# Performance work log

Measured on AMD Instinct MI355X. Metric: run time of the kernel, lower is better.

Reference implementation:

```python
import jax, jax.numpy as jnp
import numpy as np

EPS = 1e-06


def setup_inputs() -> dict:
    key = jax.random.key(0)
    k0, k1, k2, k3 = jax.random.split(key, 4)
    N = 4096  # num_gaussians (64**2)
    H = W = 128
    # Gaussian centers in [-1, 1]^2 (matches the init position grid range)
    position = jax.random.uniform(k0, (1, N, 2), minval=-1.0, maxval=1.0, dtype=jnp.float32)
    # Module stores color = raw_colors + 1 and subtracts 1 at the end of forward
    color = jax.random.uniform(k1, (1, N, 3), dtype=jnp.float32) + 1.0
    # Module init is log_scale = -5; use -3 +/- noise so kernels have visible support
    log_scale = jax.random.normal(k2, (1, N, 2), dtype=jnp.float32) * 0.5 - 3.0
    rotation = jax.random.normal(k3, (1, N), dtype=jnp.float32) * 0.5
    alphas = jnp.ones((1, N), dtype=jnp.float32)
    return dict(position=position, color=color, log_scale=log_scale,
                rotation=rotation, alphas=alphas, height=H, width=W, num_active=N)


def reference(position, color, log_scale, rotation, alphas, height, width, num_active):
    """2D anisotropic Gaussian splat render (dense per-pixel evaluation).

    For every pixel p and gaussian g: rotate the offset into the gaussian
    frame, evaluate exp(-0.5 * quadratic form), weight by alpha and
    accumulate color.  Output [1, 3, H, W] minus 1 (module returns render-1).
    """
    n = num_active
    pos = position[0, :n]                       # [N, 2]
    col = color[0, :n]                          # [N, 3]
    scale = jnp.exp(log_scale[0, :n]) + EPS     # [N, 2]
    rot = rotation[0, :n]                       # [N]
    alph = alphas[0, :n]                        # [N]

    # Pixel grid in [-1, 1], x along width, y along height
    xs = jnp.linspace(-1.0, 1.0, width, dtype=pos.dtype)
    ys = jnp.linspace(-1.0, 1.0, height, dtype=pos.dtype)
    x_grid, y_grid = jnp.meshgrid(xs, ys)       # each [H, W]
    P = height * width
    px = x_grid.reshape(P, 1)                   # [P, 1]
    py = y_grid.reshape(P, 1)

    dx = px - pos[None, :, 0]                   # [P, N]
    dy = py - pos[None, :, 1]                   # [P, N]
    c = jnp.cos(rot)[None, :]
    s = jnp.sin(rot)[None, :]
    u = dx * c + dy * s                         # rotated offsets [P, N]
    v = -dx * s + dy * c

    inv_sx = 1.0 / scale[:, 0][None, :]
    inv_sy = 1.0 / scale[:, 1][None, :]
    w = jnp.exp(-0.5 * ((u * inv_sx) ** 2 + (v * inv_sy) ** 2)) * alph[None, :]  # [P, N]

    img = jnp.einsum('pn,nc->pc', w, col)       # [P, 3]
    img = img.reshape(height, width, 3).transpose(2, 0, 1)[None]  # [1, 3, H, W]
    return img - 1.0
```

## Files before the change

### kernel.cpp

```cpp
#include <hip/hip_runtime.h>
#include <math.h>

#define EPSV 1e-6f
#define TPB 256
#define SLICES 16

typedef __attribute__((ext_vector_type(16))) float f16v;


__global__ void splat_preprocess(const float* __restrict__ pos,
                                 const float* __restrict__ col,
                                 const float* __restrict__ ls,
                                 const float* __restrict__ rot,
                                 const float* __restrict__ alph,
                                 const int* __restrict__ num_active,
                                 float4* __restrict__ params,
                                 int n_total, int n_pad) {
    int g = blockIdx.x * blockDim.x + threadIdx.x;
    if (g >= n_pad) return;
    float4 o0 = make_float4(0.f, 0.f, 0.f, 0.f);
    float4 o1 = o0, o2 = o0, o3 = o0;
    int na_cnt = *num_active;
    if (g < n_total && g < na_cnt) {
        float sx = expf(ls[2 * g])     + EPSV;
        float sy = expf(ls[2 * g + 1]) + EPSV;
        float r  = rot[g];
        float c = cosf(r), s = sinf(r);
        const float K = 0.84932180028801904f;
        float iA =  K * c / sx;
        float iB =  K * s / sx;
        float iC = -K * s / sy;
        float iD =  K * c / sy;
        float px = pos[2 * g], py = pos[2 * g + 1];
        float E = -(iA * px + iB * py);
        float F = -(iC * px + iD * py);
        float a = iA * iA + iC * iC;
        float b = iB * iB + iD * iD;
        float cc = 2.0f * (iA * iB + iC * iD);
        float d = 2.0f * (iA * E + iC * F);
        float e = 2.0f * (iB * E + iD * F);
        float f = E * E + F * F;
        float al = alph[g];
        o0 = make_float4(-a, -b, -cc, -d);
        o1 = make_float4(-e, -f, al * col[3 * g], al * col[3 * g + 1]);
        o2 = make_float4(al * col[3 * g + 2], 0.f, 0.f, 0.f);
    }
    params[4 * g + 0] = o0;
    params[4 * g + 1] = o1;
    params[4 * g + 2] = o2;
    params[4 * g + 3] = o3;
}

__global__ void splat_init(float* __restrict__ out, int n) {
    int i = blockIdx.x * blockDim.x + threadIdx.x;
    if (i < n) out[i] = -1.0f;
}

__device__ __forceinline__ void eval_one(const f16v& q, float pxx, float pyy,
                                         float pxy, float px, float py,
                                         float& accr, float& accg, float& accb) {
    float t = fmaf(pxx, q[0], q[5]);
    t = fmaf(pyy, q[1], t);
    t = fmaf(pxy, q[2], t);
    t = fmaf(px,  q[3], t);
    t = fmaf(py,  q[4], t);
    float w = __builtin_amdgcn_exp2f(t);
    accr = fmaf(w, q[6], accr);
    accg = fmaf(w, q[7], accg);
    accb = fmaf(w, q[8], accb);
}

__global__ __launch_bounds__(TPB) void splat_main(
        const float* __restrict__ params,
        const int* __restrict__ hptr,
        const int* __restrict__ wptr,
        float* __restrict__ out,
        int P, int g_per_slice) {
    int p = blockIdx.x * TPB + threadIdx.x;
    int W = *wptr;
    int H = *hptr;
    float px = 0.f, py = 0.f;
    if (p < P) {
        int x = p % W;
        int y = p / W;
        px = -1.0f + (float)x * (2.0f / (float)(W - 1));
        py = -1.0f + (float)y * (2.0f / (float)(H - 1));
    }
    float pxx = px * px, pyy = py * py, pxy = px * py;

    const float* base = params + (size_t)blockIdx.y * g_per_slice * 16;
    float accr = 0.f, accg = 0.f, accb = 0.f;

    for (int g0 = 0; g0 < g_per_slice; g0 += 4) {
        const float* sp = base + (size_t)g0 * 16;
        f16v q0, q1, q2, q3;
        asm volatile("s_load_dwordx16 %0, %1, 0x0"  : "=s"(q0) : "s"(sp));
        asm volatile("s_load_dwordx16 %0, %1, 0x40" : "=s"(q1) : "s"(sp));
        asm volatile("s_load_dwordx16 %0, %1, 0x80" : "=s"(q2) : "s"(sp));
        asm volatile("s_load_dwordx16 %0, %1, 0xc0" : "=s"(q3) : "s"(sp));
        asm volatile("s_waitcnt lgkmcnt(0)"
                     : "+s"(q0), "+s"(q1), "+s"(q2), "+s"(q3));
        eval_one(q0, pxx, pyy, pxy, px, py, accr, accg, accb);
        eval_one(q1, pxx, pyy, pxy, px, py, accr, accg, accb);
        eval_one(q2, pxx, pyy, pxy, px, py, accr, accg, accb);
        eval_one(q3, pxx, pyy, pxy, px, py, accr, accg, accb);
    }

    if (p < P) {
        atomicAdd(&out[p],         accr);
        atomicAdd(&out[P + p],     accg);
        atomicAdd(&out[2 * P + p], accb);
    }
}

extern "C" void kernel_launch(void* const* d_in, const int* in_sizes, int n_in,
                              void* d_out, int out_size, void* d_ws, size_t ws_size,
                              hipStream_t stream) {
    const float* pos  = (const float*)d_in[0];
    const float* col  = (const float*)d_in[1];
    const float* ls   = (const float*)d_in[2];
    const float* rot  = (const float*)d_in[3];
    const float* alph = (const float*)d_in[4];
    const int*   hptr = (const int*)d_in[5];
    const int*   wptr = (const int*)d_in[6];
    const int*   nact = (const int*)d_in[7];

    int N = in_sizes[3];
    int P = out_size / 3;

    const int span = SLICES * 4;
    int n_pad = ((N + span - 1) / span) * span;
    int g_per_slice = n_pad / SLICES;

    float4* params = (float4*)d_ws;

    splat_preprocess<<<(n_pad + TPB - 1) / TPB, TPB, 0, stream>>>(
        pos, col, ls, rot, alph, nact, params, N, n_pad);

    splat_init<<<(out_size + TPB - 1) / TPB, TPB, 0, stream>>>(
        (float*)d_out, out_size);

    dim3 grid((P + TPB - 1) / TPB, SLICES);
    splat_main<<<grid, TPB, 0, stream>>>(
        (const float*)params, hptr, wptr, (float*)d_out, P, g_per_slice);
}
```

Baseline: 98.35 us.

## Fuse preprocessing into splat kernel with LDS params and partial-sum reduction

```diff
diff --git a/kernel.cpp b/kernel.cpp
--- a/kernel.cpp
+++ b/kernel.cpp
@@ -1,116 +1,142 @@
 #include <hip/hip_runtime.h>
+#include <hip/hip_fp16.h>
 #include <math.h>
 
 #define EPSV 1e-6f
 #define TPB 256
-#define SLICES 16
-
-typedef __attribute__((ext_vector_type(16))) float f16v;
+#define SLICES 32
+#define PPT 4
+#define GCAP 256
 
 
-__global__ void splat_preprocess(const float* __restrict__ pos,
-                                 const float* __restrict__ col,
-                                 const float* __restrict__ ls,
-                                 const float* __restrict__ rot,
-                                 const float* __restrict__ alph,
-                                 const int* __restrict__ num_active,
-                                 float4* __restrict__ params,
-                                 int n_total, int n_pad) {
-    int g = blockIdx.x * blockDim.x + threadIdx.x;
-    if (g >= n_pad) return;
-    float4 o0 = make_float4(0.f, 0.f, 0.f, 0.f);
-    float4 o1 = o0, o2 = o0, o3 = o0;
-    int na_cnt = *num_active;
-    if (g < n_total && g < na_cnt) {
-        float sx = expf(ls[2 * g])     + EPSV;
-        float sy = expf(ls[2 * g + 1]) + EPSV;
-        float r  = rot[g];
-        float c = cosf(r), s = sinf(r);
-        const float K = 0.84932180028801904f;
-        float iA =  K * c / sx;
-        float iB =  K * s / sx;
-        float iC = -K * s / sy;
-        float iD =  K * c / sy;
-        float px = pos[2 * g], py = pos[2 * g + 1];
-        float E = -(iA * px + iB * py);
-        float F = -(iC * px + iD * py);
-        float a = iA * iA + iC * iC;
-        float b = iB * iB + iD * iD;
-        float cc = 2.0f * (iA * iB + iC * iD);
-        float d = 2.0f * (iA * E + iC * F);
-        float e = 2.0f * (iB * E + iD * F);
-        float f = E * E + F * F;
-        float al = alph[g];
-        o0 = make_float4(-a, -b, -cc, -d);
-        o1 = make_float4(-e, -f, al * col[3 * g], al * col[3 * g + 1]);
-        o2 = make_float4(al * col[3 * g + 2], 0.f, 0.f, 0.f);
-    }
-    params[4 * g + 0] = o0;
-    params[4 * g + 1] = o1;
-    params[4 * g + 2] = o2;
-    params[4 * g + 3] = o3;
+__device__ __forceinline__ float pack_half2(float a, float b) {
+    __half2 h = __floats2half2_rn(a, b);
+    union { __half2 h; float f; } u; u.h = h;
+    return u.f;
 }
 
-__global__ void splat_init(float* __restrict__ out, int n) {
-    int i = blockIdx.x * blockDim.x + threadIdx.x;
-    if (i < n) out[i] = -1.0f;
+__global__ __launch_bounds__(TPB) void splat_fused(
+        const float* __restrict__ pos,
+        const float* __restrict__ col,
+        const float* __restrict__ ls,
+        const float* __restrict__ rot,
+        const float* __restrict__ alph,
+        const int* __restrict__ nact_p,
+        const int* __restrict__ hptr,
+        const int* __restrict__ wptr,
+        float* __restrict__ partial,
+        int N, int P, int g_per_slice) {
+    __shared__ float4 sh[GCAP * 2];
+
+    const int slice = blockIdx.y;
+    const int t = threadIdx.x;
+
+    int nact = *nact_p;
+    for (int j = t; j < g_per_slice; j += TPB) {
+        int g = slice * g_per_slice + j;
+        float4 o0 = make_float4(0.f, 0.f, 0.f, 0.f);
+        float4 o1 = o0;
+        if (g < N && g < nact) {
+            float sx = expf(ls[2 * g])     + EPSV;
+            float sy = expf(ls[2 * g + 1]) + EPSV;
+            float r  = rot[g];
+            float c = cosf(r), s = sinf(r);
+            const float K = 0.84932180028801904f;
+            float iA =  K * c / sx;
+            float iB =  K * s / sx;
+            float iC = -K * s / sy;
+            float iD =  K * c / sy;
+            float px = pos[2 * g], py = pos[2 * g + 1];
+            float E = -(iA * px + iB * py);
+            float F = -(iC * px + iD * py);
+            float a  = iA * iA + iC * iC;
+            float b  = iB * iB + iD * iD;
+            float cc = 2.0f * (iA * iB + iC * iD);
+            float d  = 2.0f * (iA * E + iC * F);
+            float e  = 2.0f * (iB * E + iD * F);
+            float f  = E * E + F * F;
+            float al = alph[g];
+            float cr = al * col[3 * g];
+            float cg = al * col[3 * g + 1];
+            float cb = al * col[3 * g + 2];
+            o0 = make_float4(-a, -b, -cc, -d);
+            o1 = make_float4(-e, -f, pack_half2(cr, cg), pack_half2(cb, 0.f));
+        }
+        sh[2 * j]     = o0;
+        sh[2 * j + 1] = o1;
+    }
+    __syncthreads();
+
+    const int W = *wptr;
+    const int H = *hptr;
+    const int base = blockIdx.x * (TPB * PPT);
+    float px[PPT], py[PPT], pxx[PPT], pyy[PPT], pxy[PPT];
+#pragma unroll
+    for (int k = 0; k < PPT; ++k) {
+        int p = base + t + k * TPB;
+        int x = (p < P) ? (p % W) : 0;
+        int y = (p < P) ? (p / W) : 0;
+        px[k] = -1.0f + (float)x * (2.0f / (float)(W - 1));
+        py[k] = -1.0f + (float)y * (2.0f / (float)(H - 1));
+        pxx[k] = px[k] * px[k];
+        pyy[k] = py[k] * py[k];
+        pxy[k] = px[k] * py[k];
+    }
+
+    float accr[PPT], accg[PPT], accb[PPT];
+#pragma unroll
+    for (int k = 0; k < PPT; ++k) { accr[k] = 0.f; accg[k] = 0.f; accb[k] = 0.f; }
+
+    float4 a0 = sh[0], a1 = sh[1];
+    for (int g = 0; g < g_per_slice; ++g) {
+        int gn = (g + 1 < g_per_slice) ? (g + 1) : g;
+        float4 b0 = sh[2 * gn];
+        float4 b1 = sh[2 * gn + 1];
+
+        union { float f; __half2 h; } u01, u2x;
+        u01.f = a1.z; u2x.f = a1.w;
+        float cr = __low2float(u01.h);
+        float cg = __high2float(u01.h);
+        float cb = __low2float(u2x.h);
+
+#pragma unroll
+        for (int k = 0; k < PPT; ++k) {
+            float tt = fmaf(pxx[k], a0.x, a1.y);
+            tt = fmaf(pyy[k], a0.y, tt);
+            tt = fmaf(pxy[k], a0.z, tt);
+            tt = fmaf(px[k],  a0.w, tt);
+            tt = fmaf(py[k],  a1.x, tt);
+            float w = __builtin_amdgcn_exp2f(tt);
+            accr[k] = fmaf(w, cr, accr[k]);
+            accg[k] = fmaf(w, cg, accg[k]);
+            accb[k] = fmaf(w, cb, accb[k]);
+        }
+        a0 = b0; a1 = b1;
+    }
+
+    float* dst = partial + (size_t)slice * 3 * P;
+#pragma unroll
+    for (int k = 0; k < PPT; ++k) {
+        int p = base + t + k * TPB;
+        if (p < P) {
+            dst[p]         = accr[k];
+            dst[P + p]     = accg[k];
+            dst[2 * P + p] = accb[k];
+        }
+    }
 }
 
-__device__ __forceinline__ void eval_one(const f16v& q, float pxx, float pyy,
-                                         float pxy, float px, float py,
-                                         float& accr, float& accg, float& accb) {
-    float t = fmaf(pxx, q[0], q[5]);
-    t = fmaf(pyy, q[1], t);
-    t = fmaf(pxy, q[2], t);
-    t = fmaf(px,  q[3], t);
-    t = fmaf(py,  q[4], t);
-    float w = __builtin_amdgcn_exp2f(t);
-    accr = fmaf(w, q[6], accr);
-    accg = fmaf(w, q[7], accg);
-    accb = fmaf(w, q[8], accb);
-}
-
-__global__ __launch_bounds__(TPB) void splat_main(
-        const float* __restrict__ params,
-        const int* __restrict__ hptr,
-        const int* __restrict__ wptr,
+__global__ __launch_bounds__(TPB) void splat_reduce(
+        const float* __restrict__ partial,
         float* __restrict__ out,
-        int P, int g_per_slice) {
-    int p = blockIdx.x * TPB + threadIdx.x;
-    int W = *wptr;
-    int H = *hptr;
-    float px = 0.f, py = 0.f;
-    if (p < P) {
-        int x = p % W;
-        int y = p / W;
-        px = -1.0f + (float)x * (2.0f / (float)(W - 1));
-        py = -1.0f + (float)y * (2.0f / (float)(H - 1));
-    }
-    float pxx = px * px, pyy = py * py, pxy = px * py;
-
-    const float* base = params + (size_t)blockIdx.y * g_per_slice * 16;
-    float accr = 0.f, accg = 0.f, accb = 0.f;
-
-    for (int g0 = 0; g0 < g_per_slice; g0 += 4) {
-        const float* sp = base + (size_t)g0 * 16;
-        f16v q0, q1, q2, q3;
-        asm volatile("s_load_dwordx16 %0, %1, 0x0"  : "=s"(q0) : "s"(sp));
-        asm volatile("s_load_dwordx16 %0, %1, 0x40" : "=s"(q1) : "s"(sp));
-        asm volatile("s_load_dwordx16 %0, %1, 0x80" : "=s"(q2) : "s"(sp));
-        asm volatile("s_load_dwordx16 %0, %1, 0xc0" : "=s"(q3) : "s"(sp));
-        asm volatile("s_waitcnt lgkmcnt(0)"
-                     : "+s"(q0), "+s"(q1), "+s"(q2), "+s"(q3));
-        eval_one(q0, pxx, pyy, pxy, px, py, accr, accg, accb);
-        eval_one(q1, pxx, pyy, pxy, px, py, accr, accg, accb);
-        eval_one(q2, pxx, pyy, pxy, px, py, accr, accg, accb);
-        eval_one(q3, pxx, pyy, pxy, px, py, accr, accg, accb);
-    }
-
-    if (p < P) {
-        atomicAdd(&out[p],         accr);
-        atomicAdd(&out[P + p],     accg);
-        atomicAdd(&out[2 * P + p], accb);
-    }
+        int total) {
+    int i = blockIdx.x * TPB + threadIdx.x;
+    if (i >= total) return;
+    float s = -1.0f;
+#pragma unroll
+    for (int sl = 0; sl < SLICES; ++sl)
+        s += partial[(size_t)sl * total + i];
+    out[i] = s;
 }
 
 extern "C" void kernel_launch(void* const* d_in, const int* in_sizes, int n_in,
@@ -128,19 +154,16 @@
     int N = in_sizes[3];
     int P = out_size / 3;
 
-    const int span = SLICES * 4;
-    int n_pad = ((N + span - 1) / span) * span;
-    int g_per_slice = n_pad / SLICES;
+    int g_per_slice = (N + SLICES - 1) / SLICES;
+    if (g_per_slice > GCAP) g_per_slice = GCAP;
 
-    float4* params = (float4*)d_ws;
+    float* partial = (float*)d_ws;
 
-    splat_preprocess<<<(n_pad + TPB - 1) / TPB, TPB, 0, stream>>>(
-        pos, col, ls, rot, alph, nact, params, N, n_pad);
+    int px_blocks = (P + TPB * PPT - 1) / (TPB * PPT);
+    dim3 grid(px_blocks, SLICES);
+    splat_fused<<<grid, TPB, 0, stream>>>(
+        pos, col, ls, rot, alph, nact, hptr, wptr, partial, N, P, g_per_slice);
 
-    splat_init<<<(out_size + TPB - 1) / TPB, TPB, 0, stream>>>(
-        (float*)d_out, out_size);
-
-    dim3 grid((P + TPB - 1) / TPB, SLICES);
-    splat_main<<<grid, TPB, 0, stream>>>(
-        (const float*)params, hptr, wptr, (float*)d_out, P, g_per_slice);
+    splat_reduce<<<(out_size + TPB - 1) / TPB, TPB, 0, stream>>>(
+        partial, (float*)d_out, out_size);
 }
```

After: 91.24 us. -7.2%, faster.
